# Performance work log

Hardware: AMD Instinct MI355X
Metric: run time of the kernel (lower is better)

## Reference

```python
import jax, jax.numpy as jnp
import numpy as np

B, T, I, H, C = 32, 1024, 512, 1024, 512

def setup_inputs() -> dict:
    key = jax.random.key(0)
    ks = jax.random.split(key, 9)
    s_ih = 1.0 / np.sqrt(H)
    inp = {
        "x": jax.random.normal(ks[0], (B, T, I), dtype=jnp.float32),
        # LSTMCell params (PyTorch layout: [4H, in], gate order i,f,g,o)
        "W_ih": jax.random.uniform(ks[1], (4 * H, I), minval=-s_ih, maxval=s_ih, dtype=jnp.float32),
        "W_hh": jax.random.uniform(ks[2], (4 * H, H), minval=-s_ih, maxval=s_ih, dtype=jnp.float32),
        "b_ih": jax.random.uniform(ks[3], (4 * H,), minval=-s_ih, maxval=s_ih, dtype=jnp.float32),
        "b_hh": jax.random.uniform(ks[4], (4 * H,), minval=-s_ih, maxval=s_ih, dtype=jnp.float32),
        # fc head [C, H]
        "fc_w": jax.random.uniform(ks[5], (C, H), minval=-s_ih, maxval=s_ih, dtype=jnp.float32),
        "fc_b": jax.random.uniform(ks[6], (C,), minval=-s_ih, maxval=s_ih, dtype=jnp.float32),
        # ln_hidden [H, H] (reverse=False branch)
        "ln_w": jax.random.uniform(ks[7], (H, H), minval=-s_ih, maxval=s_ih, dtype=jnp.float32),
        "ln_b": jax.random.uniform(ks[8], (H,), minval=-s_ih, maxval=s_ih, dtype=jnp.float32),
    }
    return inp

def _lstm_forward(x, W_ih, W_hh, b_ih, b_hh):
    # Pre-compute input contribution for all timesteps: [B,T,4H]
    x_gates = jnp.einsum('bti,gi->btg', x, W_ih) + b_ih
    h0 = jnp.zeros((x.shape[0], H), dtype=x.dtype)
    c0 = jnp.zeros((x.shape[0], H), dtype=x.dtype)

    def step(carry, xg_t):
        h, c = carry
        gates = xg_t + h @ W_hh.T + b_hh  # [B,4H]
        i, f, g, o = jnp.split(gates, 4, axis=-1)
        c = jax.nn.sigmoid(f) * c + jax.nn.sigmoid(i) * jnp.tanh(g)
        h = jax.nn.sigmoid(o) * jnp.tanh(c)
        return (h, c), h

    (_, _), hs = jax.lax.scan(step, (h0, c0), jnp.swapaxes(x_gates, 0, 1))  # hs: [T,B,H]
    return jnp.swapaxes(hs, 0, 1)  # [B,T,H]

def reference(x, W_ih, W_hh, b_ih, b_hh, fc_w, fc_b, ln_w, ln_b):
    outputs = _lstm_forward(x, W_ih, W_hh, b_ih, b_hh)  # [B,T,H]
    out = jnp.einsum('bth,ch->btc', outputs, fc_w) + fc_b  # [B,T,C]
    # Faithful quirk: torch.stack(outputs, 1) on a [B,T,H] tensor -> [T,B,H]
    states_t = jnp.swapaxes(outputs, 0, 1)  # [T,B,H]
    states = jnp.einsum('tbh,gh->tbg', states_t, ln_w) + ln_b  # [T,B,H]
    return (out, states)
```

## Files before the change

kernel.cpp:

```cpp
#include <hip/hip_runtime.h>
#include <stdint.h>

#define B_  32
#define T_  1024
#define I_  512
#define H_  1024
#define C_  512
#define G4H 4096
#define NWG 128

typedef __bf16 bf16x8 __attribute__((ext_vector_type(8)));
typedef float  f32x4  __attribute__((ext_vector_type(4)));
typedef unsigned long long u64;

__device__ __forceinline__ unsigned short f2bf(float f) {
    uint32_t b = __float_as_uint(f);
    b = (b + 0x7FFFu + ((b >> 16) & 1u)) >> 16;
    return (unsigned short)b;
}
__device__ __forceinline__ float sigf(float x)   { return 1.0f / (1.0f + __expf(-x)); }
__device__ __forceinline__ float tanh_f(float x) { return 2.0f / (1.0f + __expf(-2.0f * x)) - 1.0f; }

__global__ void cvt_kernel(const float* __restrict__ src, unsigned short* __restrict__ dst, int n4) {
    int i = blockIdx.x * blockDim.x + threadIdx.x;
    if (i < n4) {
        float4 v = ((const float4*)src)[i];
        ushort4 o;
        o.x = f2bf(v.x); o.y = f2bf(v.y); o.z = f2bf(v.z); o.w = f2bf(v.w);
        ((ushort4*)dst)[i] = o;
    }
}

__global__ void bias_kernel(const float* __restrict__ a, const float* __restrict__ b, float* __restrict__ o) {
    int i = blockIdx.x * blockDim.x + threadIdx.x;
    if (i < G4H) o[i] = a[i] + b[i];
}

__global__ __launch_bounds__(512, 1) void lstm_rec(
        const unsigned short* __restrict__ whh,
        const unsigned short* __restrict__ wih,
        const unsigned short* __restrict__ xb,
        const float* __restrict__ bias,
        unsigned short* __restrict__ hall,
        unsigned int* __restrict__ flags)
{
    extern __shared__ char smem[];
    unsigned short* Wlds    = (unsigned short*)smem;
    float*          scratch = (float*)(smem + 98304);
    float*          biasl   = (float*)(smem + 98304 + 32768);
    unsigned short* hstage  = (unsigned short*)(smem + 98304 + 32768 + 128);

    const int tid  = threadIdx.x;
    const int wg   = blockIdx.x;
    const int lane = tid & 63;
    const int wq   = tid >> 6;
    const int l15  = lane & 15;
    const int l4   = lane >> 4;

    for (int s = tid; s < 32 * 192; s += 512) {
        int col = s / 192, g = s % 192;
        int grow = (col >> 3) * H_ + wg * 8 + (col & 7);
        const unsigned short* src = (g < 128) ? (whh + grow * H_ + g * 8)
                                              : (wih + grow * I_ + (g - 128) * 8);
        int4 v = *(const int4*)src;
        int gd = g ^ (col & 7);
        *(int4*)(Wlds + col * 1536 + gd * 8) = v;
    }
    if (tid < 32)
        biasl[tid] = bias[(tid >> 3) * H_ + wg * 8 + (tid & 7)];
    __syncthreads();

    float c_state = 0.0f;

    for (int t = 0; t < T_; ++t) {
        f32x4 acc[2][2];
        #pragma unroll
        for (int a = 0; a < 2; a++)
            #pragma unroll
            for (int b = 0; b < 2; b++) acc[a][b] = (f32x4){0.f, 0.f, 0.f, 0.f};

        #pragma unroll
        for (int kxs = 0; kxs < 2; kxs++) {
            int kk = wq * 64 + kxs * 32 + l4 * 8;
            bf16x8 af[2];
            #pragma unroll
            for (int mt = 0; mt < 2; mt++) {
                int bb = mt * 16 + l15;
                af[mt] = *(const bf16x8*)(xb + (bb * T_ + t) * I_ + kk);
            }
            int gbase = 128 + (kk >> 3);
            bf16x8 bfr[2];
            #pragma unroll
            for (int nt = 0; nt < 2; nt++) {
                int col = nt * 16 + l15;
                int gg = gbase ^ (col & 7);
                bfr[nt] = *(const bf16x8*)(Wlds + col * 1536 + gg * 8);
            }
            #pragma unroll
            for (int mt = 0; mt < 2; mt++)
                #pragma unroll
                for (int nt = 0; nt < 2; nt++)
                    acc[mt][nt] = __builtin_amdgcn_mfma_f32_16x16x32_bf16(af[mt], bfr[nt], acc[mt][nt], 0, 0, 0);
        }

        if (t > 0) {
            if (tid < NWG) {
                unsigned int* f = flags + (t - 1) * NWG + tid;
                while (__hip_atomic_load(f, __ATOMIC_RELAXED, __HIP_MEMORY_SCOPE_AGENT) == 0u)
                    __builtin_amdgcn_s_sleep(1);
            }
            __syncthreads();
            asm volatile("" ::: "memory");
        }

        const unsigned short* hprev = hall + (size_t)t * (B_ * H_);
        #pragma unroll
        for (int khs = 0; khs < 4; khs++) {
            int kk = wq * 128 + khs * 32 + l4 * 8;
            bf16x8 af[2];
            #pragma unroll
            for (int mt = 0; mt < 2; mt++) {
                int bb = mt * 16 + l15;
                af[mt] = *(const bf16x8*)(hprev + bb * H_ + kk);
            }
            int gbase = kk >> 3;
            bf16x8 bfr[2];
            #pragma unroll
            for (int nt = 0; nt < 2; nt++) {
                int col = nt * 16 + l15;
                int gg = gbase ^ (col & 7);
                bfr[nt] = *(const bf16x8*)(Wlds + col * 1536 + gg * 8);
            }
            #pragma unroll
            for (int mt = 0; mt < 2; mt++)
                #pragma unroll
                for (int nt = 0; nt < 2; nt++)
                    acc[mt][nt] = __builtin_amdgcn_mfma_f32_16x16x32_bf16(af[mt], bfr[nt], acc[mt][nt], 0, 0, 0);
        }

        #pragma unroll
        for (int mt = 0; mt < 2; mt++)
            #pragma unroll
            for (int nt = 0; nt < 2; nt++)
                #pragma unroll
                for (int r = 0; r < 4; r++) {
                    int bb  = mt * 16 + l4 * 4 + r;
                    int col = nt * 16 + l15;
                    scratch[(wq * 32 + bb) * 32 + col] = acc[mt][nt][r];
                }
        __syncthreads();

        if (tid < 256) {
            int bb = tid >> 3, u = tid & 7;
            float p0 = biasl[u], p1 = biasl[8 + u], p2 = biasl[16 + u], p3 = biasl[24 + u];
            #pragma unroll
            for (int q = 0; q < 8; q++) {
                const float* sc = scratch + (q * 32 + bb) * 32;
                p0 += sc[u]; p1 += sc[8 + u]; p2 += sc[16 + u]; p3 += sc[24 + u];
            }
            float ig = sigf(p0), fg = sigf(p1), gg = tanh_f(p2), og = sigf(p3);
            c_state = fg * c_state + ig * gg;
            float h = og * tanh_f(c_state);
            hstage[bb * 8 + u] = f2bf(h);
        }
        __syncthreads();

        if (tid < 64) {
            int bb = tid >> 1, part = tid & 1;
            u64 q = *(u64*)(hstage + bb * 8 + part * 4);
            u64* dst = (u64*)(hall + ((size_t)(t + 1) * B_ + bb) * H_ + wg * 8 + part * 4);
            __hip_atomic_store(dst, q, __ATOMIC_RELAXED, __HIP_MEMORY_SCOPE_AGENT);
        }
        __syncthreads();
        if (tid == 0)
            __hip_atomic_store(flags + t * NWG + wg, 1u, __ATOMIC_RELAXED, __HIP_MEMORY_SCOPE_AGENT);
    }
}

template<int PERM>
__global__ __launch_bounds__(256) void gemm_bt(
        const unsigned short* __restrict__ A,
        const unsigned short* __restrict__ Bw,
        const float* __restrict__ bias,
        float* __restrict__ out)
{
    __shared__ unsigned short As[128 * 64];
    __shared__ unsigned short Bs[128 * 64];
    const int tid  = threadIdx.x;
    const int lane = tid & 63, w = tid >> 6;
    const int wm = w >> 1, wn = w & 1;
    const int mbase = blockIdx.y * 128, nbase = blockIdx.x * 128;
    const int l15 = lane & 15, l4 = lane >> 4;

    f32x4 acc[4][4];
    #pragma unroll
    for (int i = 0; i < 4; i++)
        #pragma unroll
        for (int j = 0; j < 4; j++) acc[i][j] = (f32x4){0.f, 0.f, 0.f, 0.f};

    for (int kb = 0; kb < 16; kb++) {
        __syncthreads();
        #pragma unroll
        for (int i = 0; i < 4; i++) {
            int s = i * 256 + tid;
            int row = s >> 3, g = s & 7;
            int gd = g ^ (row & 7);
            int4 va = *(const int4*)(A  + (mbase + row) * 1024 + kb * 64 + g * 8);
            *(int4*)(As + row * 64 + gd * 8) = va;
            int4 vb = *(const int4*)(Bw + (nbase + row) * 1024 + kb * 64 + g * 8);
            *(int4*)(Bs + row * 64 + gd * 8) = vb;
        }
        __syncthreads();
        #pragma unroll
        for (int kk = 0; kk < 2; kk++) {
            bf16x8 af[4], bf[4];
            #pragma unroll
            for (int mt = 0; mt < 4; mt++) {
                int row = wm * 64 + mt * 16 + l15;
                int gg = (kk * 4 + l4) ^ (row & 7);
                af[mt] = *(const bf16x8*)(As + row * 64 + gg * 8);
            }
            #pragma unroll
            for (int nt = 0; nt < 4; nt++) {
                int row = wn * 64 + nt * 16 + l15;
                int gg = (kk * 4 + l4) ^ (row & 7);
                bf[nt] = *(const bf16x8*)(Bs + row * 64 + gg * 8);
            }
            #pragma unroll
            for (int mt = 0; mt < 4; mt++)
                #pragma unroll
                for (int nt = 0; nt < 4; nt++)
                    acc[mt][nt] = __builtin_amdgcn_mfma_f32_16x16x32_bf16(af[mt], bf[nt], acc[mt][nt], 0, 0, 0);
        }
    }
    #pragma unroll
    for (int mt = 0; mt < 4; mt++)
        #pragma unroll
        for (int nt = 0; nt < 4; nt++)
            #pragma unroll
            for (int r = 0; r < 4; r++) {
                int grow = mbase + wm * 64 + mt * 16 + l4 * 4 + r;
                int gcol = nbase + wn * 64 + nt * 16 + l15;
                float v = acc[mt][nt][r] + bias[gcol];
                int idx;
                if (PERM == 1) {
                    int tt = grow >> 5, bb = grow & 31;
                    idx = (bb * 1024 + tt) * 512 + gcol;
                } else {
                    idx = grow * 1024 + gcol;
                }
                out[idx] = v;
            }
}

extern "C" void kernel_launch(void* const* d_in, const int* in_sizes, int n_in,
                              void* d_out, int out_size, void* d_ws, size_t ws_size,
                              hipStream_t stream) {
    (void)in_sizes; (void)n_in; (void)out_size; (void)ws_size;
    const float* x    = (const float*)d_in[0];
    const float* Wih  = (const float*)d_in[1];
    const float* Whh  = (const float*)d_in[2];
    const float* bih  = (const float*)d_in[3];
    const float* bhh  = (const float*)d_in[4];
    const float* fcw  = (const float*)d_in[5];
    const float* fcb  = (const float*)d_in[6];
    const float* lnw  = (const float*)d_in[7];
    const float* lnb  = (const float*)d_in[8];
    float* out = (float*)d_out;

    char* ws = (char*)d_ws;
    size_t o = 0;
    unsigned short* whh_b = (unsigned short*)(ws + o); o += 8388608;
    unsigned short* wih_b = (unsigned short*)(ws + o); o += 4194304;
    unsigned short* fcw_b = (unsigned short*)(ws + o); o += 1048576;
    unsigned short* lnw_b = (unsigned short*)(ws + o); o += 2097152;
    unsigned short* x_b   = (unsigned short*)(ws + o); o += 33554432;
    float*          bias_c = (float*)(ws + o);         o += 16384;
    unsigned short* hall  = (unsigned short*)(ws + o); o += 67174400;
    unsigned int*   flags = (unsigned int*)(ws + o);   o += 524288;

    hipMemsetAsync(flags, 0, 524288, stream);
    hipMemsetAsync(hall, 0, 65536, stream);

    cvt_kernel<<<4096,  256, 0, stream>>>(Whh, whh_b, 4194304 / 4);
    cvt_kernel<<<2048,  256, 0, stream>>>(Wih, wih_b, 2097152 / 4);
    cvt_kernel<<<512,   256, 0, stream>>>(fcw, fcw_b, 524288 / 4);
    cvt_kernel<<<1024,  256, 0, stream>>>(lnw, lnw_b, 1048576 / 4);
    cvt_kernel<<<16384, 256, 0, stream>>>(x,   x_b,   16777216 / 4);
    bias_kernel<<<16, 256, 0, stream>>>(bih, bhh, bias_c);

    const unsigned short* a0 = whh_b;
    const unsigned short* a1 = wih_b;
    const unsigned short* a2 = x_b;
    const float*          a3 = bias_c;
    unsigned short*       a4 = hall;
    unsigned int*         a5 = flags;
    void* args[6] = { (void*)&a0, (void*)&a1, (void*)&a2, (void*)&a3, (void*)&a4, (void*)&a5 };
    hipLaunchCooperativeKernel((void*)lstm_rec, dim3(NWG), dim3(512), args,
                               (unsigned)(98304 + 32768 + 128 + 512), stream);

    const unsigned short* hseq = hall + 32768;
    gemm_bt<1><<<dim3(4, 256), 256, 0, stream>>>(hseq, fcw_b, fcb, out);
    gemm_bt<2><<<dim3(8, 256), 256, 0, stream>>>(hseq, lnw_b, lnb, out + 16777216);
}
```

Before: 4.574 ms.

## Restructure LSTM step sync: per-wave flag polling, LDS atomic reduction, split publish

After: 15.11 ms. 3.3x slower.

```diff
diff --git a/kernel.cpp b/kernel.cpp
--- a/kernel.cpp
+++ b/kernel.cpp
@@ -29,6 +29,18 @@
         o.x = f2bf(v.x); o.y = f2bf(v.y); o.z = f2bf(v.z); o.w = f2bf(v.w);
         ((ushort4*)dst)[i] = o;
     }
+}
+
+__global__ void cvt_x_kernel(const float* __restrict__ src, unsigned short* __restrict__ dst) {
+    int i4 = blockIdx.x * blockDim.x + threadIdx.x;
+    int b   = i4 / (T_ * I_ / 4);
+    int rem = i4 % (T_ * I_ / 4);
+    int t   = rem / (I_ / 4);
+    int c4  = rem % (I_ / 4);
+    float4 v = ((const float4*)src)[i4];
+    ushort4 o;
+    o.x = f2bf(v.x); o.y = f2bf(v.y); o.z = f2bf(v.z); o.w = f2bf(v.w);
+    ((ushort4*)dst)[(t * B_ + b) * (I_ / 4) + c4] = o;
 }
 
 __global__ void bias_kernel(const float* __restrict__ a, const float* __restrict__ b, float* __restrict__ o) {
@@ -47,8 +59,8 @@
     extern __shared__ char smem[];
     unsigned short* Wlds    = (unsigned short*)smem;
     float*          scratch = (float*)(smem + 98304);
-    float*          biasl   = (float*)(smem + 98304 + 32768);
-    unsigned short* hstage  = (unsigned short*)(smem + 98304 + 32768 + 128);
+    float*          biasl   = (float*)(smem + 98304 + 8192);
+    unsigned short* hstage  = (unsigned short*)(smem + 98304 + 8192 + 128);
 
     const int tid  = threadIdx.x;
     const int wg   = blockIdx.x;
@@ -68,11 +80,14 @@
     }
     if (tid < 32)
         biasl[tid] = bias[(tid >> 3) * H_ + wg * 8 + (tid & 7)];
+    for (int s = tid; s < 2048; s += 512) scratch[s] = 0.0f;
     __syncthreads();
 
     float c_state = 0.0f;
 
     for (int t = 0; t < T_; ++t) {
+        float* scr = scratch + (t & 1) * 1024;
+
         f32x4 acc[2][2];
         #pragma unroll
         for (int a = 0; a < 2; a++)
@@ -86,7 +101,7 @@
             #pragma unroll
             for (int mt = 0; mt < 2; mt++) {
                 int bb = mt * 16 + l15;
-                af[mt] = *(const bf16x8*)(xb + (bb * T_ + t) * I_ + kk);
+                af[mt] = *(const bf16x8*)(xb + ((size_t)t * B_ + bb) * I_ + kk);
             }
             int gbase = 128 + (kk >> 3);
             bf16x8 bfr[2];
@@ -104,13 +119,8 @@
         }
 
         if (t > 0) {
-            if (tid < NWG) {
-                unsigned int* f = flags + (t - 1) * NWG + tid;
-                while (__hip_atomic_load(f, __ATOMIC_RELAXED, __HIP_MEMORY_SCOPE_AGENT) == 0u)
-                    __builtin_amdgcn_s_sleep(1);
-            }
-            __syncthreads();
-            asm volatile("" ::: "memory");
+            const unsigned int* fp = flags + (size_t)t * 512 + wq * 64 + lane;
+            while (__hip_atomic_load(fp, __ATOMIC_RELAXED, __HIP_MEMORY_SCOPE_AGENT) == 0u) {}
         }
 
         const unsigned short* hprev = hall + (size_t)t * (B_ * H_);
@@ -146,34 +156,38 @@
                 for (int r = 0; r < 4; r++) {
                     int bb  = mt * 16 + l4 * 4 + r;
                     int col = nt * 16 + l15;
-                    scratch[(wq * 32 + bb) * 32 + col] = acc[mt][nt][r];
+                    unsafeAtomicAdd(&scr[bb * 32 + (col ^ ((bb & 7) << 2))], acc[mt][nt][r]);
                 }
         __syncthreads();
 
         if (tid < 256) {
             int bb = tid >> 3, u = tid & 7;
-            float p0 = biasl[u], p1 = biasl[8 + u], p2 = biasl[16 + u], p3 = biasl[24 + u];
-            #pragma unroll
-            for (int q = 0; q < 8; q++) {
-                const float* sc = scratch + (q * 32 + bb) * 32;
-                p0 += sc[u]; p1 += sc[8 + u]; p2 += sc[16 + u]; p3 += sc[24 + u];
-            }
+            int sw = (bb & 7) << 2;
+            float p0 = biasl[u]      + scr[bb * 32 + ((u)      ^ sw)];
+            float p1 = biasl[8 + u]  + scr[bb * 32 + ((8 + u)  ^ sw)];
+            float p2 = biasl[16 + u] + scr[bb * 32 + ((16 + u) ^ sw)];
+            float p3 = biasl[24 + u] + scr[bb * 32 + ((24 + u) ^ sw)];
+            scr[bb * 32 + ((u)      ^ sw)] = 0.0f;
+            scr[bb * 32 + ((8 + u)  ^ sw)] = 0.0f;
+            scr[bb * 32 + ((16 + u) ^ sw)] = 0.0f;
+            scr[bb * 32 + ((24 + u) ^ sw)] = 0.0f;
             float ig = sigf(p0), fg = sigf(p1), gg = tanh_f(p2), og = sigf(p3);
             c_state = fg * c_state + ig * gg;
             float h = og * tanh_f(c_state);
             hstage[bb * 8 + u] = f2bf(h);
-        }
-        __syncthreads();
-
-        if (tid < 64) {
-            int bb = tid >> 1, part = tid & 1;
-            u64 q = *(u64*)(hstage + bb * 8 + part * 4);
-            u64* dst = (u64*)(hall + ((size_t)(t + 1) * B_ + bb) * H_ + wg * 8 + part * 4);
-            __hip_atomic_store(dst, q, __ATOMIC_RELAXED, __HIP_MEMORY_SCOPE_AGENT);
-        }
-        __syncthreads();
-        if (tid == 0)
-            __hip_atomic_store(flags + t * NWG + wg, 1u, __ATOMIC_RELAXED, __HIP_MEMORY_SCOPE_AGENT);
+
+            int w = tid >> 6, i = tid & 63;
+            if (i < 16) {
+                int pb = w * 8 + (i >> 1), part = i & 1;
+                u64 q = *(const u64*)(hstage + pb * 8 + part * 4);
+                u64* dst = (u64*)(hall + ((size_t)(t + 1) * B_ + pb) * H_ + wg * 8 + part * 4);
+                __hip_atomic_store(dst, q, __ATOMIC_RELAXED, __HIP_MEMORY_SCOPE_AGENT);
+            }
+            asm volatile("s_waitcnt vmcnt(0)" ::: "memory");
+            if (i == 0)
+                __hip_atomic_store(flags + (size_t)(t + 1) * 512 + wg * 4 + w, 1u,
+                                   __ATOMIC_RELAXED, __HIP_MEMORY_SCOPE_AGENT);
+        }
     }
 }
 
@@ -277,16 +291,16 @@
     unsigned short* x_b   = (unsigned short*)(ws + o); o += 33554432;
     float*          bias_c = (float*)(ws + o);         o += 16384;
     unsigned short* hall  = (unsigned short*)(ws + o); o += 67174400;
-    unsigned int*   flags = (unsigned int*)(ws + o);   o += 524288;
-
-    hipMemsetAsync(flags, 0, 524288, stream);
+    unsigned int*   flags = (unsigned int*)(ws + o);   o += 2099200;
+
+    hipMemsetAsync(flags, 0, 2099200, stream);
     hipMemsetAsync(hall, 0, 65536, stream);
 
     cvt_kernel<<<4096,  256, 0, stream>>>(Whh, whh_b, 4194304 / 4);
     cvt_kernel<<<2048,  256, 0, stream>>>(Wih, wih_b, 2097152 / 4);
     cvt_kernel<<<512,   256, 0, stream>>>(fcw, fcw_b, 524288 / 4);
     cvt_kernel<<<1024,  256, 0, stream>>>(lnw, lnw_b, 1048576 / 4);
-    cvt_kernel<<<16384, 256, 0, stream>>>(x,   x_b,   16777216 / 4);
+    cvt_x_kernel<<<16384, 256, 0, stream>>>(x, x_b);
     bias_kernel<<<16, 256, 0, stream>>>(bih, bhh, bias_c);
 
     const unsigned short* a0 = whh_b;
@@ -297,7 +311,7 @@
     unsigned int*         a5 = flags;
     void* args[6] = { (void*)&a0, (void*)&a1, (void*)&a2, (void*)&a3, (void*)&a4, (void*)&a5 };
     hipLaunchCooperativeKernel((void*)lstm_rec, dim3(NWG), dim3(512), args,
-                               (unsigned)(98304 + 32768 + 128 + 512), stream);
+                               (unsigned)(98304 + 8192 + 128 + 512), stream);
 
     const unsigned short* hseq = hall + 32768;
     gemm_bt<1><<<dim3(4, 256), 256, 0, stream>>>(hseq, fcw_b, fcb, out);
```

## Confine LSTM recurrence to one XCD with register-resident W_hh and precomputed x-gates

Applied to the files above, without the earlier changes.

Measured after the change: 9.414 ms. 106% more time.

```diff
diff --git a/kernel.cpp b/kernel.cpp
--- a/kernel.cpp
+++ b/kernel.cpp
@@ -7,7 +7,6 @@
 #define H_  1024
 #define C_  512
 #define G4H 4096
-#define NWG 128
 
 typedef __bf16 bf16x8 __attribute__((ext_vector_type(8)));
 typedef float  f32x4  __attribute__((ext_vector_type(4)));
@@ -17,6 +16,9 @@
     uint32_t b = __float_as_uint(f);
     b = (b + 0x7FFFu + ((b >> 16) & 1u)) >> 16;
     return (unsigned short)b;
+}
+__device__ __forceinline__ float bf2f(unsigned short v) {
+    return __uint_as_float(((uint32_t)v) << 16);
 }
 __device__ __forceinline__ float sigf(float x)   { return 1.0f / (1.0f + __expf(-x)); }
 __device__ __forceinline__ float tanh_f(float x) { return 2.0f / (1.0f + __expf(-2.0f * x)) - 1.0f; }
@@ -36,7 +38,294 @@
     if (i < G4H) o[i] = a[i] + b[i];
 }
 
-__global__ __launch_bounds__(512, 1) void lstm_rec(
+__global__ void fill_kernel(u64* __restrict__ dst, u64 val, size_t n) {
+    size_t i = (size_t)blockIdx.x * blockDim.x + threadIdx.x;
+    if (i < n)
+        __hip_atomic_store(dst + i, val, __ATOMIC_RELAXED, __HIP_MEMORY_SCOPE_AGENT);
+}
+
+__global__ void init_kernel(u64* __restrict__ ctrl, u64* __restrict__ flags, u64* __restrict__ hall0) {
+    int i = blockIdx.x * blockDim.x + threadIdx.x;
+    if (i < 5)
+        __hip_atomic_store(ctrl + i, (i == 4) ? ~0ull : 0ull, __ATOMIC_RELAXED, __HIP_MEMORY_SCOPE_AGENT);
+    if (i < 128)
+        __hip_atomic_store(flags + i, 0ull, __ATOMIC_RELAXED, __HIP_MEMORY_SCOPE_AGENT);
+    if (i < 8192)
+        __hip_atomic_store(hall0 + i, 0ull, __ATOMIC_RELAXED, __HIP_MEMORY_SCOPE_AGENT);
+}
+
+__global__ __launch_bounds__(256) void xg_gemm(
+        const unsigned short* __restrict__ A,
+        const unsigned short* __restrict__ Bw,
+        unsigned short* __restrict__ out)
+{
+    __shared__ unsigned short As[128 * 64];
+    __shared__ unsigned short Bs[128 * 64];
+    const int tid  = threadIdx.x;
+    const int lane = tid & 63, w = tid >> 6;
+    const int wm = w >> 1, wn = w & 1;
+    const int mbase = blockIdx.y * 128, nbase = blockIdx.x * 128;
+    const int l15 = lane & 15, l4 = lane >> 4;
+
+    f32x4 acc[4][4];
+    #pragma unroll
+    for (int i = 0; i < 4; i++)
+        #pragma unroll
+        for (int j = 0; j < 4; j++) acc[i][j] = (f32x4){0.f, 0.f, 0.f, 0.f};
+
+    for (int kb = 0; kb < 8; kb++) {
+        __syncthreads();
+        #pragma unroll
+        for (int i = 0; i < 4; i++) {
+            int s = i * 256 + tid;
+            int row = s >> 3, g = s & 7;
+            int gd = g ^ (row & 7);
+            int4 va = *(const int4*)(A  + (size_t)(mbase + row) * 512 + kb * 64 + g * 8);
+            *(int4*)(As + row * 64 + gd * 8) = va;
+            int4 vb = *(const int4*)(Bw + (size_t)(nbase + row) * 512 + kb * 64 + g * 8);
+            *(int4*)(Bs + row * 64 + gd * 8) = vb;
+        }
+        __syncthreads();
+        #pragma unroll
+        for (int kk = 0; kk < 2; kk++) {
+            bf16x8 af[4], bf[4];
+            #pragma unroll
+            for (int mt = 0; mt < 4; mt++) {
+                int row = wm * 64 + mt * 16 + l15;
+                int gg = (kk * 4 + l4) ^ (row & 7);
+                af[mt] = *(const bf16x8*)(As + row * 64 + gg * 8);
+            }
+            #pragma unroll
+            for (int nt = 0; nt < 4; nt++) {
+                int row = wn * 64 + nt * 16 + l15;
+                int gg = (kk * 4 + l4) ^ (row & 7);
+                bf[nt] = *(const bf16x8*)(Bs + row * 64 + gg * 8);
+            }
+            #pragma unroll
+            for (int mt = 0; mt < 4; mt++)
+                #pragma unroll
+                for (int nt = 0; nt < 4; nt++)
+                    acc[mt][nt] = __builtin_amdgcn_mfma_f32_16x16x32_bf16(af[mt], bf[nt], acc[mt][nt], 0, 0, 0);
+        }
+    }
+    #pragma unroll
+    for (int mt = 0; mt < 4; mt++)
+        #pragma unroll
+        for (int nt = 0; nt < 4; nt++)
+            #pragma unroll
+            for (int r = 0; r < 4; r++) {
+                int grow = mbase + wm * 64 + mt * 16 + l4 * 4 + r;
+                int gcol = nbase + wn * 64 + nt * 16 + l15;
+                int b = grow >> 10, t = grow & 1023;
+                out[((size_t)t * B_ + b) * G4H + gcol] = f2bf(acc[mt][nt][r]);
+            }
+}
+
+__global__ __launch_bounds__(512, 2) void lstm_xcd(
+        const unsigned short* __restrict__ whh,
+        const unsigned short* __restrict__ xg,
+        const float* __restrict__ bias,
+        unsigned short* __restrict__ hall,
+        unsigned short* __restrict__ hall2,
+        int* __restrict__ ctrl,
+        int* __restrict__ flags)
+{
+    extern __shared__ char smem[];
+    unsigned short* hlds   = (unsigned short*)smem;
+    float*          scratch = (float*)(smem + 65536);
+    unsigned short* xstage = (unsigned short*)(smem + 131072);
+    int*            s_slot = (int*)(smem + 139264);
+
+    const int tid  = threadIdx.x;
+    const int lane = tid & 63;
+    const int wq   = tid >> 6;
+    const int l15  = lane & 15;
+    const int l4   = lane >> 4;
+
+    if (tid == 0) {
+        int myxcd;
+        asm volatile("s_getreg_b32 %0, hwreg(HW_REG_XCC_ID, 0, 4)" : "=s"(myxcd));
+        myxcd &= 7;
+        int idx = __hip_atomic_fetch_add(&ctrl[myxcd], 1, __ATOMIC_RELAXED, __HIP_MEMORY_SCOPE_AGENT);
+        if (idx == 31) {
+            int e = -1;
+            __hip_atomic_compare_exchange_strong(&ctrl[8], &e, myxcd,
+                __ATOMIC_RELAXED, __ATOMIC_RELAXED, __HIP_MEMORY_SCOPE_AGENT);
+        }
+        int w;
+        for (;;) {
+            w = __hip_atomic_load(&ctrl[8], __ATOMIC_RELAXED, __HIP_MEMORY_SCOPE_AGENT);
+            if (w != -1) break;
+            __builtin_amdgcn_s_sleep(8);
+        }
+        *s_slot = (w == myxcd && idx < 32) ? idx : -1;
+    }
+    __syncthreads();
+    const int slot = *s_slot;
+    if (slot < 0) return;
+
+    const int kw = wq >> 1, cw = wq & 1;
+
+    bf16x8 wf[8][4];
+    #pragma unroll
+    for (int ks = 0; ks < 8; ks++)
+        #pragma unroll
+        for (int nt = 0; nt < 4; nt++) {
+            int c = cw * 64 + nt * 16 + l15;
+            int grow = (c >> 5) * 1024 + slot * 32 + (c & 31);
+            wf[ks][nt] = *(const bf16x8*)(whh + (size_t)grow * 1024 + kw * 256 + ks * 32 + l4 * 8);
+        }
+
+    const int u  = tid & 31;
+    const int b0 = tid >> 5;
+    const int b1 = b0 + 16;
+    const int U  = slot * 32 + u;
+    const float bi = bias[U], bff = bias[1024 + U], bg = bias[2048 + U], bo = bias[3072 + U];
+    float c0 = 0.f, c1 = 0.f;
+
+    const int id0 = wq * 128 + lane, id1 = id0 + 64;
+    #define XG_SRC(tt, id) (const u64*)(xg + ((size_t)(tt) * B_ + ((id) >> 5)) * G4H \
+                           + (((id) >> 3) & 3) * 1024 + slot * 32 + ((id) & 7) * 4)
+    u64 xr0 = *XG_SRC(0, id0);
+    u64 xr1 = *XG_SRC(0, id1);
+
+    const int swl15 = l15 & 7;
+
+    for (int t = 0; t < T_; ++t) {
+        if (t > 0 && wq == 0) {
+            u64* fp = (u64*)flags + lane * 2;
+            const int need = t;
+            for (;;) {
+                u64 a = __hip_atomic_load(fp,     __ATOMIC_RELAXED, __HIP_MEMORY_SCOPE_AGENT);
+                u64 b = __hip_atomic_load(fp + 1, __ATOMIC_RELAXED, __HIP_MEMORY_SCOPE_AGENT);
+                bool ok = ((int)(uint32_t)(a & 0xffffffffu) >= need) &&
+                          ((int)(uint32_t)(a >> 32)         >= need) &&
+                          ((int)(uint32_t)(b & 0xffffffffu) >= need) &&
+                          ((int)(uint32_t)(b >> 32)         >= need);
+                if (__all(ok)) break;
+                __builtin_amdgcn_s_sleep(1);
+            }
+            asm volatile("" ::: "memory");
+        }
+        __syncthreads();
+
+        {
+            const unsigned short* hsrc = hall + (size_t)t * (B_ * H_);
+            int b = lane >> 1, seg = lane & 1;
+            #pragma unroll
+            for (int j = 0; j < 8; j++) {
+                int g = wq * 16 + seg * 8 + j;
+                int4 v = *(const int4*)(hsrc + b * 1024 + g * 8);
+                *(int4*)((char*)hlds + b * 2048 + ((g ^ (b & 7)) << 4)) = v;
+            }
+        }
+        *(u64*)((char*)xstage + (size_t)id0 * 8) = xr0;
+        *(u64*)((char*)xstage + (size_t)id1 * 8) = xr1;
+        {
+            int tn = (t + 1 < T_) ? t + 1 : T_ - 1;
+            xr0 = *XG_SRC(tn, id0);
+            xr1 = *XG_SRC(tn, id1);
+        }
+        __syncthreads();
+
+        f32x4 acc[2][4];
+        #pragma unroll
+        for (int i = 0; i < 2; i++)
+            #pragma unroll
+            for (int j = 0; j < 4; j++) acc[i][j] = (f32x4){0.f, 0.f, 0.f, 0.f};
+
+        #pragma unroll
+        for (int ks = 0; ks < 8; ks++) {
+            int g = kw * 32 + ks * 4 + l4;
+            bf16x8 a0 = *(const bf16x8*)((char*)hlds + l15 * 2048        + ((g ^ swl15) << 4));
+            bf16x8 a1 = *(const bf16x8*)((char*)hlds + (16 + l15) * 2048 + ((g ^ swl15) << 4));
+            #pragma unroll
+            for (int nt = 0; nt < 4; nt++) {
+                acc[0][nt] = __builtin_amdgcn_mfma_f32_16x16x32_bf16(a0, wf[ks][nt], acc[0][nt], 0, 0, 0);
+                acc[1][nt] = __builtin_amdgcn_mfma_f32_16x16x32_bf16(a1, wf[ks][nt], acc[1][nt], 0, 0, 0);
+            }
+        }
+
+        #pragma unroll
+        for (int mt = 0; mt < 2; mt++)
+            #pragma unroll
+            for (int nt = 0; nt < 4; nt++)
+                #pragma unroll
+                for (int r = 0; r < 4; r++) {
+                    int b = mt * 16 + l4 * 4 + r;
+                    int c = cw * 64 + nt * 16 + l15;
+                    scratch[((kw * 32 + b) << 7) + (c ^ (((b >> 2) & 1) << 4))] = acc[mt][nt][r];
+                }
+        __syncthreads();
+
+        unsigned short* hd = hall + (size_t)(t + 1) * (B_ * H_);
+        unsigned short hv0, hv1;
+        {
+            int sw = ((b0 >> 2) & 1) << 4;
+            float pi = bi + bf2f(xstage[b0 * 128 + u]);
+            float pf = bff + bf2f(xstage[b0 * 128 + 32 + u]);
+            float pg = bg + bf2f(xstage[b0 * 128 + 64 + u]);
+            float po = bo + bf2f(xstage[b0 * 128 + 96 + u]);
+            #pragma unroll
+            for (int q = 0; q < 4; q++) {
+                const float* sc = scratch + ((q * 32 + b0) << 7);
+                pi += sc[(u) ^ sw]; pf += sc[(32 + u) ^ sw];
+                pg += sc[(64 + u) ^ sw]; po += sc[(96 + u) ^ sw];
+            }
+            float ig = sigf(pi), fg = sigf(pf), gg = tanh_f(pg), og = sigf(po);
+            c0 = fg * c0 + ig * gg;
+            hv0 = f2bf(og * tanh_f(c0));
+            hd[b0 * 1024 + U] = hv0;
+        }
+        {
+            int sw = ((b1 >> 2) & 1) << 4;
+            float pi = bi + bf2f(xstage[b1 * 128 + u]);
+            float pf = bff + bf2f(xstage[b1 * 128 + 32 + u]);
+            float pg = bg + bf2f(xstage[b1 * 128 + 64 + u]);
+            float po = bo + bf2f(xstage[b1 * 128 + 96 + u]);
+            #pragma unroll
+            for (int q = 0; q < 4; q++) {
+                const float* sc = scratch + ((q * 32 + b1) << 7);
+                pi += sc[(u) ^ sw]; pf += sc[(32 + u) ^ sw];
+                pg += sc[(64 + u) ^ sw]; po += sc[(96 + u) ^ sw];
+            }
+            float ig = sigf(pi), fg = sigf(pf), gg = tanh_f(pg), og = sigf(po);
+            c1 = fg * c1 + ig * gg;
+            hv1 = f2bf(og * tanh_f(c1));
+            hd[b1 * 1024 + U] = hv1;
+        }
+        asm volatile("s_waitcnt vmcnt(0)" ::: "memory");
+        if (lane == 0)
+            __hip_atomic_store(&flags[slot * 8 + wq], t + 1, __ATOMIC_RELAXED, __HIP_MEMORY_SCOPE_AGENT);
+    }
+
+    if (wq == 0) {
+        u64* fp = (u64*)flags + lane * 2;
+        for (;;) {
+            u64 a = __hip_atomic_load(fp,     __ATOMIC_RELAXED, __HIP_MEMORY_SCOPE_AGENT);
+            u64 b = __hip_atomic_load(fp + 1, __ATOMIC_RELAXED, __HIP_MEMORY_SCOPE_AGENT);
+            bool ok = ((int)(uint32_t)(a & 0xffffffffu) >= T_) &&
+                      ((int)(uint32_t)(a >> 32)         >= T_) &&
+                      ((int)(uint32_t)(b & 0xffffffffu) >= T_) &&
+                      ((int)(uint32_t)(b >> 32)         >= T_);
+            if (__all(ok)) break;
+            __builtin_amdgcn_s_sleep(1);
+        }
+        asm volatile("" ::: "memory");
+    }
+    __syncthreads();
+    {
+        const u64* hs64 = (const u64*)(hall + 32768);
+        u64* hd64 = (u64*)(hall2 + 32768);
+        size_t base = (size_t)slot * 262144;
+        for (int j = tid; j < 262144; j += 512) {
+            u64 v = hs64[base + j];
+            __hip_atomic_store(&hd64[base + j], v, __ATOMIC_RELAXED, __HIP_MEMORY_SCOPE_AGENT);
+        }
+    }
+}
+
+__global__ __launch_bounds__(512, 1) void lstm_fb(
         const unsigned short* __restrict__ whh,
         const unsigned short* __restrict__ wih,
         const unsigned short* __restrict__ xb,
@@ -86,7 +375,7 @@
             #pragma unroll
             for (int mt = 0; mt < 2; mt++) {
                 int bb = mt * 16 + l15;
-                af[mt] = *(const bf16x8*)(xb + (bb * T_ + t) * I_ + kk);
+                af[mt] = *(const bf16x8*)(xb + ((size_t)bb * T_ + t) * I_ + kk);
             }
             int gbase = 128 + (kk >> 3);
             bf16x8 bfr[2];
@@ -104,8 +393,8 @@
         }
 
         if (t > 0) {
-            if (tid < NWG) {
-                unsigned int* f = flags + (t - 1) * NWG + tid;
+            if (tid < 128) {
+                unsigned int* f = flags + (size_t)(t - 1) * 128 + tid;
                 while (__hip_atomic_load(f, __ATOMIC_RELAXED, __HIP_MEMORY_SCOPE_AGENT) == 0u)
                     __builtin_amdgcn_s_sleep(1);
             }
@@ -173,7 +462,8 @@
         }
         __syncthreads();
         if (tid == 0)
-            __hip_atomic_store(flags + t * NWG + wg, 1u, __ATOMIC_RELAXED, __HIP_MEMORY_SCOPE_AGENT);
+            __hip_atomic_store(flags + (size_t)t * 128 + wg, 1u,
+                               __ATOMIC_RELAXED, __HIP_MEMORY_SCOPE_AGENT);
     }
 }
 
@@ -205,9 +495,9 @@
             int s = i * 256 + tid;
             int row = s >> 3, g = s & 7;
             int gd = g ^ (row & 7);
-            int4 va = *(const int4*)(A  + (mbase + row) * 1024 + kb * 64 + g * 8);
+            int4 va = *(const int4*)(A  + (size_t)(mbase + row) * 1024 + kb * 64 + g * 8);
             *(int4*)(As + row * 64 + gd * 8) = va;
-            int4 vb = *(const int4*)(Bw + (nbase + row) * 1024 + kb * 64 + g * 8);
+            int4 vb = *(const int4*)(Bw + (size_t)(nbase + row) * 1024 + kb * 64 + g * 8);
             *(int4*)(Bs + row * 64 + gd * 8) = vb;
         }
         __syncthreads();
@@ -256,7 +546,7 @@
 extern "C" void kernel_launch(void* const* d_in, const int* in_sizes, int n_in,
                               void* d_out, int out_size, void* d_ws, size_t ws_size,
                               hipStream_t stream) {
-    (void)in_sizes; (void)n_in; (void)out_size; (void)ws_size;
+    (void)in_sizes; (void)n_in; (void)out_size;
     const float* x    = (const float*)d_in[0];
     const float* Wih  = (const float*)d_in[1];
     const float* Whh  = (const float*)d_in[2];
@@ -274,32 +564,60 @@
     unsigned short* wih_b = (unsigned short*)(ws + o); o += 4194304;
     unsigned short* fcw_b = (unsigned short*)(ws + o); o += 1048576;
     unsigned short* lnw_b = (unsigned short*)(ws + o); o += 2097152;
-    unsigned short* x_b   = (unsigned short*)(ws + o); o += 33554432;
     float*          bias_c = (float*)(ws + o);         o += 16384;
     unsigned short* hall  = (unsigned short*)(ws + o); o += 67174400;
-    unsigned int*   flags = (unsigned int*)(ws + o);   o += 524288;
-
-    hipMemsetAsync(flags, 0, 524288, stream);
-    hipMemsetAsync(hall, 0, 65536, stream);
+    unsigned short* hall2 = (unsigned short*)(ws + o); o += 67174400;
+    int*            ctrl  = (int*)(ws + o);            o += 64;
+    int*            flagsX = (int*)(ws + o);           o += 1024;
+    unsigned short* xgbuf = (unsigned short*)(ws + o); o += 268435456;
+    const int use_xg = (ws_size >= o) ? 1 : 0;
 
     cvt_kernel<<<4096,  256, 0, stream>>>(Whh, whh_b, 4194304 / 4);
     cvt_kernel<<<2048,  256, 0, stream>>>(Wih, wih_b, 2097152 / 4);
     cvt_kernel<<<512,   256, 0, stream>>>(fcw, fcw_b, 524288 / 4);
     cvt_kernel<<<1024,  256, 0, stream>>>(lnw, lnw_b, 1048576 / 4);
-    cvt_kernel<<<16384, 256, 0, stream>>>(x,   x_b,   16777216 / 4);
     bias_kernel<<<16, 256, 0, stream>>>(bih, bhh, bias_c);
 
-    const unsigned short* a0 = whh_b;
-    const unsigned short* a1 = wih_b;
-    const unsigned short* a2 = x_b;
-    const float*          a3 = bias_c;
-    unsigned short*       a4 = hall;
-    unsigned int*         a5 = flags;
-    void* args[6] = { (void*)&a0, (void*)&a1, (void*)&a2, (void*)&a3, (void*)&a4, (void*)&a5 };
-    hipLaunchCooperativeKernel((void*)lstm_rec, dim3(NWG), dim3(512), args,
-                               (unsigned)(98304 + 32768 + 128 + 512), stream);
-
-    const unsigned short* hseq = hall + 32768;
-    gemm_bt<1><<<dim3(4, 256), 256, 0, stream>>>(hseq, fcw_b, fcb, out);
-    gemm_bt<2><<<dim3(8, 256), 256, 0, stream>>>(hseq, lnw_b, lnb, out + 16777216);
-}
+    if (use_xg) {
+        unsigned short* x_b = hall;
+        cvt_kernel<<<16384, 256, 0, stream>>>(x, x_b, 16777216 / 4);
+        xg_gemm<<<dim3(32, 256), 256, 0, stream>>>(x_b, wih_b, xgbuf);
+        init_kernel<<<32, 256, 0, stream>>>((u64*)ctrl, (u64*)flagsX, (u64*)hall);
+
+        const unsigned short* a0 = whh_b;
+        const unsigned short* a1 = xgbuf;
+        const float*          a2 = bias_c;
+        unsigned short*       a3 = hall;
+        unsigned short*       a4 = hall2;
+        int*                  a5 = ctrl;
+        int*                  a6 = flagsX;
+        void* args[7] = { (void*)&a0, (void*)&a1, (void*)&a2, (void*)&a3,
+                          (void*)&a4, (void*)&a5, (void*)&a6 };
+        hipLaunchCooperativeKernel((void*)lstm_xcd, dim3(256), dim3(512), args,
+                                   (unsigned)(139264 + 16), stream);
+
+        const unsigned short* hseq = hall2 + 32768;
+        gemm_bt<1><<<dim3(4, 256), 256, 0, stream>>>(hseq, fcw_b, fcb, out);
+        gemm_bt<2><<<dim3(8, 256), 256, 0, stream>>>(hseq, lnw_b, lnb, out + 16777216);
+    } else {
+        unsigned short* x_b   = (unsigned short*)(ws + 82919424);
+        unsigned int*   flags = (unsigned int*)(ws + 82919424 + 33554432);
+        hipMemsetAsync(flags, 0, 524288, stream);
+        hipMemsetAsync(hall, 0, 65536, stream);
+        cvt_kernel<<<16384, 256, 0, stream>>>(x, x_b, 16777216 / 4);
+
+        const unsigned short* a0 = whh_b;
+        const unsigned short* a1 = wih_b;
+        const unsigned short* a2 = x_b;
+        const float*          a3 = bias_c;
+        unsigned short*       a4 = hall;
+        unsigned int*         a5 = flags;
+        void* args[6] = { (void*)&a0, (void*)&a1, (void*)&a2, (void*)&a3, (void*)&a4, (void*)&a5 };
+        hipLaunchCooperativeKernel((void*)lstm_fb, dim3(128), dim3(512), args,
+                                   (unsigned)131712, stream);
+
+        const unsigned short* hseq = hall + 32768;
+        gemm_bt<1><<<dim3(4, 256), 256, 0, stream>>>(hseq, fcw_b, fcb, out);
+        gemm_bt<2><<<dim3(8, 256), 256, 0, stream>>>(hseq, lnw_b, lnb, out + 16777216);
+    }
+}
```
